# Optimization experiments

Measured on AMD Instinct MI355X. Metric: run time of the kernel, lower is better.

The kernel has to match this reference:

```python
import jax, jax.numpy as jnp
import numpy as np

# Layer hyperparams (from TwoLayerSNN.__init__)
L1 = dict(thresh=0.5, tau_mem=10.0, tau_syn=5.0, dt=1.0, grad_type='gaussian', lens=0.5, gamma=1.0, hight=0.15)
L2 = dict(thresh=1.0, tau_mem=20.0, tau_syn=10.0, dt=1.0, grad_type='multi_gaussian', lens=0.4, gamma=1.2, hight=0.2)

B, T, D, H, O = 256, 1000, 32, 200, 2


def _gaussian(x, mu, sigma):
    return jnp.exp(-((x - mu) ** 2) / (2.0 * sigma ** 2)) / (jnp.sqrt(2.0 * jnp.pi) * sigma)


def make_spike(grad_type, lens, gamma, hight):
    """Heaviside forward, surrogate-gradient backward."""
    @jax.custom_vjp
    def spike(x):
        return (x > 0).astype(x.dtype)

    def fwd(x):
        return spike(x), x

    def bwd(x, g):
        if grad_type == 'gaussian':
            temp = _gaussian(x, 0.0, lens)
        else:  # multi_gaussian
            scale = 6.0
            temp = (_gaussian(x, 0.0, lens) * (1.0 + hight)
                    - _gaussian(x, lens, scale * lens) * hight
                    - _gaussian(x, -lens, scale * lens) * hight)
        return (g * temp * gamma,)

    spike.defvjp(fwd, bwd)
    return spike

_spike1 = make_spike(L1['grad_type'], L1['lens'], L1['gamma'], L1['hight'])
_spike2 = make_spike(L2['grad_type'], L2['lens'], L2['gamma'], L2['hight'])


def setup_inputs() -> dict:
    key = jax.random.key(0)
    k1, k2, k3 = jax.random.split(key, 3)
    x = jax.random.normal(k1, (B, T, D), dtype=jnp.float32)
    w1 = jax.random.normal(k2, (D, H), dtype=jnp.float32) / np.sqrt(D)
    w2 = jax.random.normal(k3, (H, O), dtype=jnp.float32) / np.sqrt(H)
    return {"x": x, "w1": w1, "w2": w2}


def _snn_forward(x, w1, w2):
    dtype = x.dtype
    # decay constants (compile-time scalars)
    a_syn1 = np.exp(-L1['dt'] / L1['tau_syn']); a_mem1 = np.exp(-L1['dt'] / L1['tau_mem'])
    in_sc1 = (1.0 - a_syn1) * L1['tau_syn']
    a_syn2 = np.exp(-L2['dt'] / L2['tau_syn']); a_mem2 = np.exp(-L2['dt'] / L2['tau_mem'])
    in_sc2 = (1.0 - a_syn2) * L2['tau_syn']
    th1, th2 = L1['thresh'], L2['thresh']

    b = x.shape[0]
    zeros = lambda n: jnp.zeros((b, n), dtype=dtype)
    init = (zeros(w1.shape[1]), zeros(w1.shape[1]), zeros(w2.shape[1]), zeros(w2.shape[1]))

    def step(carry, x_t):
        syn1, mem1, syn2, mem2 = carry
        syn1 = a_syn1 * syn1 + in_sc1 * (x_t @ w1)
        mem1 = a_mem1 * mem1 + (1.0 - a_mem1) * syn1
        s1 = _spike1(mem1 - th1)
        mem1 = mem1 - s1 * th1  # soft reset
        syn2 = a_syn2 * syn2 + in_sc2 * (s1 @ w2)
        mem2 = a_mem2 * mem2 + (1.0 - a_mem2) * syn2
        s2 = _spike2(mem2 - th2)
        mem2 = mem2 - s2 * th2  # soft reset
        return (syn1, mem1, syn2, mem2), (s1, mem1, s2, mem2)

    xt = jnp.swapaxes(x, 0, 1)  # [T, B, D]
    _, (s1, m1, s2, m2) = jax.lax.scan(step, init, xt)
    # accumulate post-reset mem2 for t>0, averaged over seq_length
    seq_len = x.shape[1]
    output = jnp.sum(m2[1:], axis=0) / seq_len  # [B, O]
    to_bt = lambda a: jnp.swapaxes(a, 0, 1)  # [B, T, ...]
    return output, to_bt(s1), to_bt(m1), to_bt(s2), to_bt(m2)


def reference(x, w1, w2):
    return _snn_forward(x, w1, w2)
```

## Files before the change

### kernel.cpp

```cpp
#include <hip/hip_runtime.h>


constexpr int TB = 256;
constexpr int TT = 1000;
constexpr int DD = 32;
constexpr int HH = 200;
constexpr int OO = 2;
constexpr int CH = 64;
constexpr int NCH = (TT + CH - 1) / CH;
constexpr int SC = 8;
constexpr int NSC = TT / SC;

typedef float v2f __attribute__((ext_vector_type(2)));

__device__ __forceinline__ v2f pk_fma(v2f a, v2f b, v2f c) {
#if __has_builtin(__builtin_elementwise_fma)
    return __builtin_elementwise_fma(a, b, c);
#else
    v2f r; r.x = fmaf(a.x, b.x, c.x); r.y = fmaf(a.y, b.y, c.y); return r;
#endif
}

template <int CTRL>
__device__ __forceinline__ float dpp_add(float v) {
    int t = __builtin_amdgcn_update_dpp(0, __float_as_int(v), CTRL, 0xf, 0xf, true);
    return v + __int_as_float(t);
}

__device__ __forceinline__ float read_lane_f(float v, int l) {
    return __int_as_float(__builtin_amdgcn_readlane(__float_as_int(v), l));
}

__device__ __forceinline__ void block_sync_lds() {
    asm volatile("s_waitcnt lgkmcnt(0)" ::: "memory");
    __builtin_amdgcn_s_barrier();
    asm volatile("" ::: "memory");
}

__global__ __launch_bounds__(576, 1)
void snn_fwd(const float* __restrict__ x,
             const float* __restrict__ w1,
             const float* __restrict__ w2,
             float* __restrict__ out)
{
    const int b    = blockIdx.x;
    const int tid  = threadIdx.x;
    const int lane = tid & 63;
    const int wid  = tid >> 6;
    const bool is_cons = (wid < 4);
    const bool is_prod = (wid >= 4 && wid < 8);
    const int ptid = tid - 256;
    const bool act = is_cons && (tid < HH);

    float* __restrict__ outp = out;
    float* __restrict__ s1o  = out + (size_t)TB * OO;
    float* __restrict__ m1o  = s1o + (size_t)TB * TT * HH;
    float* __restrict__ s2o  = m1o + (size_t)TB * TT * HH;
    float* __restrict__ m2o  = s2o + (size_t)TB * TT * OO;

    const float A_SYN1 = (float)0.8187307530779818;
    const float IN_SC1 = (float)((1.0 - 0.8187307530779818) * 5.0);
    const float A_MEM1 = (float)0.9048374180359595;
    const float B_MEM1 = (float)(1.0 - 0.9048374180359595);
    const float TH1    = 0.5f;
    const float A_SYN2 = (float)0.9048374180359595;
    const float IN_SC2 = (float)((1.0 - 0.9048374180359595) * 10.0);
    const float A_MEM2 = (float)0.9512294245007140;
    const float B_MEM2 = (float)(1.0 - 0.9512294245007140);
    const float TH2    = 1.0f;

    __shared__ float4 xls[2][CH * DD / 4];
    __shared__ float  dotb[2][SC][HH];
    __shared__ __align__(16) float2 partv[2][SC][16];

    const float* __restrict__ xb = x + (size_t)b * TT * DD;

    const int ph   = (wid - 4) * 50 + lane;
    const bool pact = is_prod && (lane < 50);
    v2f w1e[DD / 4], w1o[DD / 4];
#pragma unroll
    for (int i = 0; i < DD / 4; ++i) {
        w1e[i] = pact ? v2f{w1[(4 * i) * HH + ph],     w1[(4 * i + 1) * HH + ph]} : v2f{0.f, 0.f};
        w1o[i] = pact ? v2f{w1[(4 * i + 2) * HH + ph], w1[(4 * i + 3) * HH + ph]} : v2f{0.f, 0.f};
    }
    const float w2x = act ? w2[tid * OO + 0] : 0.0f;
    const float w2y = act ? w2[tid * OO + 1] : 0.0f;

    if (is_cons) {
        const float4* g = (const float4*)xb;
        xls[0][2 * tid]     = g[2 * tid];
        xls[0][2 * tid + 1] = g[2 * tid + 1];
    }
    block_sync_lds();

    auto produce = [&](int j) {
        const int tj = j * SC;
        const float4* xq = &xls[(tj >> 6) & 1][(tj & 63) * (DD / 4)];
#pragma unroll
        for (int s = 0; s < SC; ++s) {
            const float4 X0 = xq[s * 8 + 0], X1 = xq[s * 8 + 1];
            const float4 X2 = xq[s * 8 + 2], X3 = xq[s * 8 + 3];
            const float4 X4 = xq[s * 8 + 4], X5 = xq[s * 8 + 5];
            const float4 X6 = xq[s * 8 + 6], X7 = xq[s * 8 + 7];
            v2f A01 = {0.f, 0.f}, A23 = {0.f, 0.f};
            A01 = pk_fma(v2f{X0.x, X0.y}, w1e[0], A01);
            A23 = pk_fma(v2f{X0.z, X0.w}, w1o[0], A23);
            A01 = pk_fma(v2f{X1.x, X1.y}, w1e[1], A01);
            A23 = pk_fma(v2f{X1.z, X1.w}, w1o[1], A23);
            A01 = pk_fma(v2f{X2.x, X2.y}, w1e[2], A01);
            A23 = pk_fma(v2f{X2.z, X2.w}, w1o[2], A23);
            A01 = pk_fma(v2f{X3.x, X3.y}, w1e[3], A01);
            A23 = pk_fma(v2f{X3.z, X3.w}, w1o[3], A23);
            A01 = pk_fma(v2f{X4.x, X4.y}, w1e[4], A01);
            A23 = pk_fma(v2f{X4.z, X4.w}, w1o[4], A23);
            A01 = pk_fma(v2f{X5.x, X5.y}, w1e[5], A01);
            A23 = pk_fma(v2f{X5.z, X5.w}, w1o[5], A23);
            A01 = pk_fma(v2f{X6.x, X6.y}, w1e[6], A01);
            A23 = pk_fma(v2f{X6.z, X6.w}, w1o[6], A23);
            A01 = pk_fma(v2f{X7.x, X7.y}, w1e[7], A01);
            A23 = pk_fma(v2f{X7.z, X7.w}, w1o[7], A23);
            const float dotv = __fadd_rn(__fadd_rn(A01.x, A01.y),
                                         __fadd_rn(A23.x, A23.y));
            if (pact) dotb[j & 1][s][ph] = dotv;
        }
    };

    if (is_prod) produce(0);
    block_sync_lds();

    float syn1 = 0.0f, mem1 = 0.0f;
    float syn2x = 0.0f, syn2y = 0.0f, mem2x = 0.0f, mem2y = 0.0f;
    double accx = 0.0, accy = 0.0;

    float4 pr0 = make_float4(0.f, 0.f, 0.f, 0.f);
    float4 pr1 = make_float4(0.f, 0.f, 0.f, 0.f);
    int nfl4 = 0;

    float* __restrict__ s1p = s1o + (size_t)b * TT * HH + tid;
    float* __restrict__ m1p = m1o + (size_t)b * TT * HH + tid;
    float2* __restrict__ s2p = (float2*)(s2o + (size_t)b * TT * OO);
    float2* __restrict__ m2p = (float2*)(m2o + (size_t)b * TT * OO);

    auto l2_chunk = [&](int j) {
        const int g = lane >> 4;
        const int p = lane & 15;
#pragma unroll
        for (int half = 0; half < 2; ++half) {
            const float2 v = partv[j & 1][4 * half + g][p];
            float cxv = v.x, cyv = v.y;
            cxv = dpp_add<0x111>(cxv); cyv = dpp_add<0x111>(cyv);
            cxv = dpp_add<0x112>(cxv); cyv = dpp_add<0x112>(cyv);
            cxv = dpp_add<0x114>(cxv); cyv = dpp_add<0x114>(cyv);
            cxv = dpp_add<0x118>(cxv); cyv = dpp_add<0x118>(cyv);
#pragma unroll
            for (int gg = 0; gg < 4; ++gg) {
                const float dx = read_lane_f(cxv, 16 * gg + 15);
                const float dy = read_lane_f(cyv, 16 * gg + 15);
                syn2x = __fadd_rn(__fmul_rn(A_SYN2, syn2x), __fmul_rn(IN_SC2, dx));
                syn2y = __fadd_rn(__fmul_rn(A_SYN2, syn2y), __fmul_rn(IN_SC2, dy));
                mem2x = __fadd_rn(__fmul_rn(A_MEM2, mem2x), __fmul_rn(B_MEM2, syn2x));
                mem2y = __fadd_rn(__fmul_rn(A_MEM2, mem2y), __fmul_rn(B_MEM2, syn2y));
                const float s2x = (mem2x - TH2 > 0.0f) ? 1.0f : 0.0f;
                const float s2y = (mem2y - TH2 > 0.0f) ? 1.0f : 0.0f;
                mem2x = __fsub_rn(mem2x, __fmul_rn(s2x, TH2));
                mem2y = __fsub_rn(mem2y, __fmul_rn(s2y, TH2));
                const int t = j * SC + 4 * half + gg;
                if (tid == 512) {
                    s2p[t] = make_float2(s2x, s2y);
                    m2p[t] = make_float2(mem2x, mem2y);
                }
                if (t > 0) { accx += (double)mem2x; accy += (double)mem2y; }
            }
        }
    };

    for (int sc = 0; sc < NSC; ++sc) {
        const int t0   = sc * SC;
        const int c    = t0 >> 6;
        const int cpos = t0 & 63;

        if (is_cons) {
            float D[SC];
#pragma unroll
            for (int s = 0; s < SC; ++s) D[s] = dotb[sc & 1][s][tid];

#pragma unroll
            for (int s = 0; s < SC; ++s) {
                const float dot = D[s];
                syn1 = __fadd_rn(__fmul_rn(A_SYN1, syn1), __fmul_rn(IN_SC1, dot));
                mem1 = __fadd_rn(__fmul_rn(A_MEM1, mem1), __fmul_rn(B_MEM1, syn1));
                const float s1v = (mem1 - TH1 > 0.0f) ? 1.0f : 0.0f;
                mem1 = __fsub_rn(mem1, __fmul_rn(s1v, TH1));

                if (act) {
                    s1p[(size_t)(t0 + s) * HH] = s1v;
                    m1p[(size_t)(t0 + s) * HH] = mem1;
                }

                float cx = s1v * w2x;
                float cy = s1v * w2y;
                cx = dpp_add<0x111>(cx); cy = dpp_add<0x111>(cy);
                cx = dpp_add<0x112>(cx); cy = dpp_add<0x112>(cy);
                cx = dpp_add<0x114>(cx); cy = dpp_add<0x114>(cy);
                cx = dpp_add<0x118>(cx); cy = dpp_add<0x118>(cy);
                if ((lane & 15) == 15)
                    partv[sc & 1][s][wid * 4 + (lane >> 4)] = make_float2(cx, cy);
            }
        } else if (is_prod) {
            if (cpos == 0 && c + 1 < NCH) {
                const int nst = (CH < TT - (c + 1) * CH) ? CH : (TT - (c + 1) * CH);
                nfl4 = nst * DD / 4;
                const float4* g = (const float4*)(xb + (size_t)(c + 1) * CH * DD);
                if (2 * ptid     < nfl4) pr0 = g[2 * ptid];
                if (2 * ptid + 1 < nfl4) pr1 = g[2 * ptid + 1];
            }

            if (sc + 1 < NSC) produce(sc + 1);

            if (cpos == 48 && c + 1 < NCH) {
                if (2 * ptid     < nfl4) xls[(c + 1) & 1][2 * ptid]     = pr0;
                if (2 * ptid + 1 < nfl4) xls[(c + 1) & 1][2 * ptid + 1] = pr1;
            }
        } else {
            if (sc > 0) l2_chunk(sc - 1);
        }

        block_sync_lds();
    }

    if (wid == 8) {
        l2_chunk(NSC - 1);
        if (tid == 512) {
            outp[b * OO + 0] = (float)accx / 1000.0f;
            outp[b * OO + 1] = (float)accy / 1000.0f;
        }
    }
}

extern "C" void kernel_launch(void* const* d_in, const int* in_sizes, int n_in,
                              void* d_out, int out_size, void* d_ws, size_t ws_size,
                              hipStream_t stream) {
    const float* x  = (const float*)d_in[0];
    const float* w1 = (const float*)d_in[1];
    const float* w2 = (const float*)d_in[2];
    float* out = (float*)d_out;

    dim3 grid(TB), block(576);
    hipLaunchKernelGGL(snn_fwd, grid, block, 0, stream, x, w1, w2, out);
}
```

Before: 186.9 us.

## Enlarge per-sync timestep chunk to cut block barriers, restage x in 40-step chunks

Raises the number of timesteps processed between block barriers from 8 to 20 and shrinks the x staging chunk from 64 to 40 steps, so each chunk is exactly two produce batches. The x prefetch is now loaded and written to LDS within the same superstep, replacing the delayed write. The layer-2 recurrence is rewritten with packed two-wide vectors, with contraction disabled to keep rounding unchanged. Fewer barriers are meant to reduce sync overhead across the 1000-step serial scan, at the cost of larger LDS buffers, more registers per wave and longer per-superstep critical paths.

```diff
diff --git a/kernel.cpp b/kernel.cpp
--- a/kernel.cpp
+++ b/kernel.cpp
@@ -6,10 +6,11 @@
 constexpr int DD = 32;
 constexpr int HH = 200;
 constexpr int OO = 2;
-constexpr int CH = 64;
-constexpr int NCH = (TT + CH - 1) / CH;
-constexpr int SC = 8;
+constexpr int CH = 40;
+constexpr int NCH = TT / CH;
+constexpr int SC = 20;
 constexpr int NSC = TT / SC;
+constexpr int XF4 = CH * DD / 4;
 
 typedef float v2f __attribute__((ext_vector_type(2)));
 
@@ -69,7 +70,7 @@
     const float B_MEM2 = (float)(1.0 - 0.9512294245007140);
     const float TH2    = 1.0f;
 
-    __shared__ float4 xls[2][CH * DD / 4];
+    __shared__ float4 xls[2][XF4];
     __shared__ float  dotb[2][SC][HH];
     __shared__ __align__(16) float2 partv[2][SC][16];
 
@@ -88,14 +89,13 @@
 
     if (is_cons) {
         const float4* g = (const float4*)xb;
-        xls[0][2 * tid]     = g[2 * tid];
-        xls[0][2 * tid + 1] = g[2 * tid + 1];
+        if (2 * tid     < XF4) xls[0][2 * tid]     = g[2 * tid];
+        if (2 * tid + 1 < XF4) xls[0][2 * tid + 1] = g[2 * tid + 1];
     }
     block_sync_lds();
 
     auto produce = [&](int j) {
-        const int tj = j * SC;
-        const float4* xq = &xls[(tj >> 6) & 1][(tj & 63) * (DD / 4)];
+        const float4* xq = &xls[(j >> 1) & 1][(j & 1) * SC * (DD / 4)];
 #pragma unroll
         for (int s = 0; s < SC; ++s) {
             const float4 X0 = xq[s * 8 + 0], X1 = xq[s * 8 + 1];
@@ -129,12 +129,13 @@
     block_sync_lds();
 
     float syn1 = 0.0f, mem1 = 0.0f;
-    float syn2x = 0.0f, syn2y = 0.0f, mem2x = 0.0f, mem2y = 0.0f;
     double accx = 0.0, accy = 0.0;
-
-    float4 pr0 = make_float4(0.f, 0.f, 0.f, 0.f);
-    float4 pr1 = make_float4(0.f, 0.f, 0.f, 0.f);
-    int nfl4 = 0;
+    v2f syn2 = {0.f, 0.f}, mem2 = {0.f, 0.f};
+    const v2f A2v  = {A_SYN2, A_SYN2};
+    const v2f SC2v = {IN_SC2, IN_SC2};
+    const v2f AM2v = {A_MEM2, A_MEM2};
+    const v2f BM2v = {B_MEM2, B_MEM2};
+    const v2f TH2v = {TH2, TH2};
 
     float* __restrict__ s1p = s1o + (size_t)b * TT * HH + tid;
     float* __restrict__ m1p = m1o + (size_t)b * TT * HH + tid;
@@ -142,10 +143,11 @@
     float2* __restrict__ m2p = (float2*)(m2o + (size_t)b * TT * OO);
 
     auto l2_chunk = [&](int j) {
+#pragma clang fp contract(off)
         const int g = lane >> 4;
         const int p = lane & 15;
 #pragma unroll
-        for (int half = 0; half < 2; ++half) {
+        for (int half = 0; half < SC / 4; ++half) {
             const float2 v = partv[j & 1][4 * half + g][p];
             float cxv = v.x, cyv = v.y;
             cxv = dpp_add<0x111>(cxv); cyv = dpp_add<0x111>(cyv);
@@ -154,30 +156,28 @@
             cxv = dpp_add<0x118>(cxv); cyv = dpp_add<0x118>(cyv);
 #pragma unroll
             for (int gg = 0; gg < 4; ++gg) {
-                const float dx = read_lane_f(cxv, 16 * gg + 15);
-                const float dy = read_lane_f(cyv, 16 * gg + 15);
-                syn2x = __fadd_rn(__fmul_rn(A_SYN2, syn2x), __fmul_rn(IN_SC2, dx));
-                syn2y = __fadd_rn(__fmul_rn(A_SYN2, syn2y), __fmul_rn(IN_SC2, dy));
-                mem2x = __fadd_rn(__fmul_rn(A_MEM2, mem2x), __fmul_rn(B_MEM2, syn2x));
-                mem2y = __fadd_rn(__fmul_rn(A_MEM2, mem2y), __fmul_rn(B_MEM2, syn2y));
-                const float s2x = (mem2x - TH2 > 0.0f) ? 1.0f : 0.0f;
-                const float s2y = (mem2y - TH2 > 0.0f) ? 1.0f : 0.0f;
-                mem2x = __fsub_rn(mem2x, __fmul_rn(s2x, TH2));
-                mem2y = __fsub_rn(mem2y, __fmul_rn(s2y, TH2));
+                const v2f d = {read_lane_f(cxv, 16 * gg + 15),
+                               read_lane_f(cyv, 16 * gg + 15)};
+                syn2 = (A2v * syn2) + (SC2v * d);
+                mem2 = (AM2v * mem2) + (BM2v * syn2);
+                const float s2x = (mem2.x - TH2 > 0.0f) ? 1.0f : 0.0f;
+                const float s2y = (mem2.y - TH2 > 0.0f) ? 1.0f : 0.0f;
+                const v2f s2v = {s2x, s2y};
+                mem2 = mem2 - (s2v * TH2v);
                 const int t = j * SC + 4 * half + gg;
                 if (tid == 512) {
                     s2p[t] = make_float2(s2x, s2y);
-                    m2p[t] = make_float2(mem2x, mem2y);
+                    m2p[t] = make_float2(mem2.x, mem2.y);
                 }
-                if (t > 0) { accx += (double)mem2x; accy += (double)mem2y; }
+                if (t > 0) { accx += (double)mem2.x; accy += (double)mem2.y; }
             }
         }
     };
 
     for (int sc = 0; sc < NSC; ++sc) {
         const int t0   = sc * SC;
-        const int c    = t0 >> 6;
-        const int cpos = t0 & 63;
+        const int c    = t0 / CH;
+        const int cpos = t0 % CH;
 
         if (is_cons) {
             float D[SC];
@@ -207,19 +207,19 @@
                     partv[sc & 1][s][wid * 4 + (lane >> 4)] = make_float2(cx, cy);
             }
         } else if (is_prod) {
-            if (cpos == 0 && c + 1 < NCH) {
-                const int nst = (CH < TT - (c + 1) * CH) ? CH : (TT - (c + 1) * CH);
-                nfl4 = nst * DD / 4;
+            float4 pr0, pr1;
+            const bool stage = (cpos == 0 && c + 1 < NCH);
+            if (stage) {
                 const float4* g = (const float4*)(xb + (size_t)(c + 1) * CH * DD);
-                if (2 * ptid     < nfl4) pr0 = g[2 * ptid];
-                if (2 * ptid + 1 < nfl4) pr1 = g[2 * ptid + 1];
+                if (2 * ptid     < XF4) pr0 = g[2 * ptid];
+                if (2 * ptid + 1 < XF4) pr1 = g[2 * ptid + 1];
             }
 
             if (sc + 1 < NSC) produce(sc + 1);
 
-            if (cpos == 48 && c + 1 < NCH) {
-                if (2 * ptid     < nfl4) xls[(c + 1) & 1][2 * ptid]     = pr0;
-                if (2 * ptid + 1 < nfl4) xls[(c + 1) & 1][2 * ptid + 1] = pr1;
+            if (stage) {
+                if (2 * ptid     < XF4) xls[(c + 1) & 1][2 * ptid]     = pr0;
+                if (2 * ptid + 1 < XF4) xls[(c + 1) & 1][2 * ptid + 1] = pr1;
             }
         } else {
             if (sc > 0) l2_chunk(sc - 1);
```

New measurement: 184.1 us. No clear change (-1.5%).
